# Kernel optimization log

Measured on AMD Instinct MI355X. Metric: run time of the kernel, lower is better.

The kernel has to match this reference:

```python
import jax, jax.numpy as jnp
import numpy as np

NUM_SAMPLED = 8192
NUM_CLASSES = 50000
DIM = 512
BATCH = 8192


def _log_uniform_expected(ids, num_sampled, num_classes):
    # log-uniform sampler probability: P(c) = (log(c+2) - log(c+1)) / log(V+1)
    c = ids.astype(jnp.float32)
    p = (jnp.log(c + 2.0) - jnp.log(c + 1.0)) / jnp.log(float(num_classes + 1))
    # expected count under unique sampling of num_sampled candidates (as in TF)
    return -jnp.expm1(float(num_sampled) * jnp.log1p(-p))


def setup_inputs() -> dict:
    key = jax.random.key(0)
    k1, k2, k3, k4, k5 = jax.random.split(key, 5)
    inputs = jax.random.normal(k1, (BATCH, DIM), jnp.float32)
    labels = jax.random.randint(k2, (BATCH, 1), 0, NUM_CLASSES)
    kernel = jax.random.uniform(k3, (NUM_CLASSES, DIM), jnp.float32, -0.05, 0.05)
    bias = jax.random.uniform(k4, (NUM_CLASSES,), jnp.float32, -0.05, 0.05)
    sampled = jax.random.randint(k5, (NUM_SAMPLED,), 0, NUM_CLASSES)
    return {"inputs": inputs, "labels": labels, "kernel": kernel,
            "bias": bias, "sampled": sampled}


def reference(inputs, labels, kernel, bias, sampled):
    # tf.nn.sampled_softmax_loss (train branch), num_true=1,
    # log-uniform sampler, remove_accidental_hits=True.
    labels_flat = labels[:, 0]

    # true logits: gather one weight row per example, dot with input
    w_true = kernel[labels_flat]                      # [B, D]
    b_true = bias[labels_flat]                        # [B]
    true_logits = jnp.einsum('bd,bd->b', inputs, w_true) + b_true
    true_logits = true_logits - jnp.log(
        _log_uniform_expected(labels_flat, NUM_SAMPLED, NUM_CLASSES))

    # sampled logits: gather S candidate rows, small matmul [B,D]x[D,S]
    w_samp = kernel[sampled]                          # [S, D]
    b_samp = bias[sampled]                            # [S]
    sampled_logits = jnp.einsum('bd,sd->bs', inputs, w_samp) + b_samp[None, :]
    sampled_logits = sampled_logits - jnp.log(
        _log_uniform_expected(sampled, NUM_SAMPLED, NUM_CLASSES))

    # remove accidental hits: mask sampled candidates that equal the true label
    hits = labels_flat[:, None] == sampled[None, :]   # [B, S]
    sampled_logits = jnp.where(hits, -1e9, sampled_logits)

    # softmax CE with the true class at column 0
    logits = jnp.concatenate([true_logits[:, None], sampled_logits], axis=1)
    loss = jax.nn.logsumexp(logits, axis=1) - logits[:, 0]  # [B]
    return loss
```

## Files before the change

kernel.cpp:

```cpp
#include <hip/hip_runtime.h>
#include <hip/hip_bf16.h>
#include <cstdint>
#include <cstddef>

#define BATCH   8192
#define NSAMP   8192
#define DIM     512
#define NCLASS  50000
#define HBINS   50176

typedef __attribute__((ext_vector_type(8))) short bf16x8;
typedef __attribute__((ext_vector_type(4))) float f32x4;

__device__ __forceinline__ float neg_log_expected(int c) {
    double p = log1p(1.0 / (double)(c + 1)) / log((double)(NCLASS + 1));
    double e = -expm1((double)NSAMP * log1p(-p));
    return (float)(-log(e));
}

__device__ __forceinline__ unsigned short f2bf(float f) {
    __hip_bfloat16 h = __float2bfloat16(f);
    return *reinterpret_cast<unsigned short*>(&h);
}

__device__ __forceinline__ void gload_lds16(const void* g, void* l) {
    __builtin_amdgcn_global_load_lds(
        (const __attribute__((address_space(1))) void*)g,
        (__attribute__((address_space(3))) void*)l, 16, 0, 0);
}

__global__ void k_zero(int* __restrict__ hist) {
    hist[blockIdx.x * 1024 + threadIdx.x] = 0;
}
__global__ void k_hist(const int* __restrict__ sampled, int* __restrict__ hist) {
    atomicAdd(&hist[sampled[blockIdx.x * 1024 + threadIdx.x]], 1);
}
__global__ void k_scan1(const int* __restrict__ hist, int* __restrict__ btot) {
    int b = blockIdx.x, t = threadIdx.x;
    int c = b * 196 + t;
    int x = (t < 196 && c < NCLASS && hist[c] > 0) ? 1 : 0;
    int lane = t & 63, wv = t >> 6;
    #pragma unroll
    for (int off = 32; off; off >>= 1) x += __shfl_down(x, off, 64);
    __shared__ int ws[4];
    if (lane == 0) ws[wv] = x;
    __syncthreads();
    if (t == 0) btot[b] = ws[0] + ws[1] + ws[2] + ws[3];
}
__global__ void k_scan2(const int* __restrict__ btot, int* __restrict__ boff,
                        int* __restrict__ meta) {
    int t = threadIdx.x;
    int v = btot[t];
    int lane = t & 63, wv = t >> 6;
    int x = v;
    #pragma unroll
    for (int off = 1; off < 64; off <<= 1) {
        int y = __shfl_up(x, off, 64);
        if (lane >= off) x += y;
    }
    __shared__ int ws[4];
    if (lane == 63) ws[wv] = x;
    __syncthreads();
    int base = 0;
    for (int w = 0; w < wv; ++w) base += ws[w];
    boff[t] = base + x - v;
    if (t == 255) {
        int D = base + x;
        meta[0] = D;
        meta[1] = (D + 127) & ~127;
    }
}
__global__ void k_scatter(const int* __restrict__ hist, const int* __restrict__ boff,
                          int* __restrict__ didx) {
    int b = blockIdx.x, t = threadIdx.x;
    int c = b * 196 + t;
    int ind = (t < 196 && c < NCLASS && hist[c] > 0) ? 1 : 0;
    int lane = t & 63, wv = t >> 6;
    int x = ind;
    #pragma unroll
    for (int off = 1; off < 64; off <<= 1) {
        int y = __shfl_up(x, off, 64);
        if (lane >= off) x += y;
    }
    __shared__ int ws[4];
    if (lane == 63) ws[wv] = x;
    __syncthreads();
    int base = boff[b];
    for (int w = 0; w < wv; ++w) base += ws[w];
    if (ind) didx[base + x - 1] = c;
}

__global__ void k_prep(const float* __restrict__ inputs, const int* __restrict__ labels,
                       const float* __restrict__ W, const float* __restrict__ bias,
                       const int* __restrict__ hist, const int* __restrict__ didx,
                       const int* __restrict__ meta,
                       __hip_bfloat16* __restrict__ Abf, __hip_bfloat16* __restrict__ Bbf,
                       float* __restrict__ adj,
                       float* __restrict__ true_logit, float* __restrict__ row_sum) {
    int bid = blockIdx.x;
    int t   = threadIdx.x;
    if (bid < BATCH) {
        int row = bid;
        float4 v = reinterpret_cast<const float4*>(inputs + (size_t)row * DIM)[t];
        ushort4 u;
        u.x = f2bf(v.x); u.y = f2bf(v.y); u.z = f2bf(v.z); u.w = f2bf(v.w);
        reinterpret_cast<ushort4*>(Abf + (size_t)row * DIM)[t] = u;

        int lbl = labels[row];
        float4 w = reinterpret_cast<const float4*>(W + (size_t)lbl * DIM)[t];
        float dot = v.x * w.x + v.y * w.y + v.z * w.z + v.w * w.w;
        #pragma unroll
        for (int off = 32; off; off >>= 1) dot += __shfl_down(dot, off, 64);
        __shared__ float red[2];
        if ((t & 63) == 0) red[t >> 6] = dot;
        __syncthreads();
        if (t == 0) {
            float tl = red[0] + red[1] + bias[lbl] + neg_log_expected(lbl);
            true_logit[row] = tl;
            row_sum[row]    = (1.0f - (float)hist[lbl]) * __expf(tl);
        }
    } else {
        int s = bid - BATCH;
        int D = meta[0], padD = meta[1];
        if (s >= padD) return;
        if (s < D) {
            int idx = didx[s];
            float4 v = reinterpret_cast<const float4*>(W + (size_t)idx * DIM)[t];
            ushort4 u;
            u.x = f2bf(v.x); u.y = f2bf(v.y); u.z = f2bf(v.z); u.w = f2bf(v.w);
            reinterpret_cast<ushort4*>(Bbf + (size_t)s * DIM)[t] = u;
            if (t == 0)
                adj[s] = bias[idx] + neg_log_expected(idx) + logf((float)hist[idx]);
        } else {
            ushort4 z; z.x = z.y = z.z = z.w = 0;
            reinterpret_cast<ushort4*>(Bbf + (size_t)s * DIM)[t] = z;
            if (t == 0) adj[s] = -100000.0f;
        }
    }
}

__global__ __launch_bounds__(256, 4) void k_gemm(
    const __hip_bfloat16* __restrict__ A, const __hip_bfloat16* __restrict__ B,
    const float* __restrict__ adj, const int* __restrict__ labels,
    const int* __restrict__ meta, float* __restrict__ row_sum) {
    __shared__ alignas(16) __hip_bfloat16 Asm[2][128 * 32];
    __shared__ alignas(16) __hip_bfloat16 Bsm[2][128 * 32];
    __shared__ float tsum[2][128];

    const int tid  = threadIdx.x;
    const int wave = tid >> 6;
    const int lane = tid & 63;
    const int wr   = wave >> 1;
    const int wc   = wave & 1;

    const int bid  = blockIdx.x;
    const int xcd  = bid & 7;
    const int u    = bid >> 3;
    const int rb   = xcd * 8 + (u & 7);
    const int cgrp = u >> 3;
    const int brow = rb * 128;

    const int nct = meta[1] >> 7;
    const int ntl = (nct > cgrp) ? (((nct - cgrp - 1) >> 4) + 1) : 0;
    if (ntl == 0) return;
    const int nsteps = ntl << 4;

    const int srow = lane >> 2;
    const int sg   = (lane & 3) ^ ((lane >> 3) & 3);
    const int rsel = lane & 15;
    const int koff = ((lane >> 4) ^ ((lane >> 1) & 3)) * 8;

    f32x4 acc[4][4];
    #pragma unroll
    for (int m = 0; m < 4; ++m)
        #pragma unroll
        for (int n = 0; n < 4; ++n)
            acc[m][n] = (f32x4){0.f, 0.f, 0.f, 0.f};

    auto stage = [&](int g) {
        const int buf = g & 1, t = g >> 4, kt = g & 15;
        const int bcol = (cgrp + t * 16) << 7;
        #pragma unroll
        for (int i = 0; i < 2; ++i) {
            const __hip_bfloat16* gA =
                A + (size_t)(brow + wave * 32 + i * 16 + srow) * DIM + kt * 32 + sg * 8;
            gload_lds16(gA, &Asm[buf][(wave * 32 + i * 16) * 32]);
            const __hip_bfloat16* gB =
                B + (size_t)(bcol + wave * 32 + i * 16 + srow) * DIM + kt * 32 + sg * 8;
            gload_lds16(gB, &Bsm[buf][(wave * 32 + i * 16) * 32]);
        }
    };

    auto body = [&](int buf) {
        bf16x8 a[4], b[4];
        #pragma unroll
        for (int m = 0; m < 4; ++m)
            a[m] = *reinterpret_cast<const bf16x8*>(
                &Asm[buf][(wr * 64 + m * 16 + rsel) * 32 + koff]);
        #pragma unroll
        for (int n = 0; n < 4; ++n)
            b[n] = *reinterpret_cast<const bf16x8*>(
                &Bsm[buf][(wc * 64 + n * 16 + rsel) * 32 + koff]);
        #pragma unroll
        for (int m = 0; m < 4; ++m)
            #pragma unroll
            for (int n = 0; n < 4; ++n)
                acc[m][n] = __builtin_amdgcn_mfma_f32_16x16x32_bf16(a[m], b[n], acc[m][n], 0, 0, 0);
    };

    auto epi = [&](int i) {
        const int bcol = (cgrp + i * 16) << 7;
        float aadj[4];
        #pragma unroll
        for (int n = 0; n < 4; ++n) aadj[n] = adj[bcol + wc * 64 + n * 16 + rsel];
        #pragma unroll
        for (int m = 0; m < 4; ++m) {
            #pragma unroll
            for (int r = 0; r < 4; ++r) {
                int lr = wr * 64 + m * 16 + (lane >> 4) * 4 + r;
                float part = 0.f;
                #pragma unroll
                for (int n = 0; n < 4; ++n)
                    part += __expf(acc[m][n][r] + aadj[n]);
                part += __shfl_xor(part, 1, 16);
                part += __shfl_xor(part, 2, 16);
                part += __shfl_xor(part, 4, 16);
                part += __shfl_xor(part, 8, 16);
                if (rsel == 0) tsum[wc][lr] = part;
            }
        }
        __syncthreads();
        if (tid < 128)
            atomicAdd(&row_sum[brow + tid], tsum[0][tid] + tsum[1][tid]);
        #pragma unroll
        for (int m = 0; m < 4; ++m)
            #pragma unroll
            for (int n = 0; n < 4; ++n)
                acc[m][n] = (f32x4){0.f, 0.f, 0.f, 0.f};
    };

    stage(0);
    __syncthreads();

    #pragma unroll 1
    for (int g = 0; g < nsteps; ++g) {
        if (g + 1 < nsteps) stage(g + 1);
        body(g & 1);
        if ((g & 15) == 15) epi(g >> 4);
        __syncthreads();
    }
}

__global__ void k_final(const float* __restrict__ row_sum,
                        const float* __restrict__ true_logit,
                        float* __restrict__ loss) {
    int i = blockIdx.x * blockDim.x + threadIdx.x;
    loss[i] = logf(row_sum[i]) - true_logit[i];
}

extern "C" void kernel_launch(void* const* d_in, const int* in_sizes, int n_in,
                              void* d_out, int out_size, void* d_ws, size_t ws_size,
                              hipStream_t stream) {
    const float* inputs  = (const float*)d_in[0];
    const int*   labels  = (const int*)d_in[1];
    const float* W       = (const float*)d_in[2];
    const float* bias    = (const float*)d_in[3];
    const int*   sampled = (const int*)d_in[4];
    float*       loss    = (float*)d_out;

    char* ws = (char*)d_ws;
    __hip_bfloat16* Abf = (__hip_bfloat16*)ws;
    __hip_bfloat16* Bbf = (__hip_bfloat16*)(ws + (size_t)BATCH * DIM * 2);
    size_t off = (size_t)(BATCH + NSAMP) * DIM * 2;
    float* adj        = (float*)(ws + off);            off += NSAMP * 4;
    float* true_logit = (float*)(ws + off);            off += BATCH * 4;
    float* row_sum    = (float*)(ws + off);            off += BATCH * 4;
    int*   hist       = (int*)(ws + off);              off += HBINS * 4;
    int*   btot       = (int*)(ws + off);              off += 256 * 4;
    int*   boff       = (int*)(ws + off);              off += 256 * 4;
    int*   meta       = (int*)(ws + off);              off += 16;
    int*   didx       = (int*)(ws + off);              off += NSAMP * 4;

    hipLaunchKernelGGL(k_zero,    dim3(HBINS / 1024), dim3(1024), 0, stream, hist);
    hipLaunchKernelGGL(k_hist,    dim3(NSAMP / 1024), dim3(1024), 0, stream, sampled, hist);
    hipLaunchKernelGGL(k_scan1,   dim3(256), dim3(256), 0, stream, hist, btot);
    hipLaunchKernelGGL(k_scan2,   dim3(1),   dim3(256), 0, stream, btot, boff, meta);
    hipLaunchKernelGGL(k_scatter, dim3(256), dim3(256), 0, stream, hist, boff, didx);
    hipLaunchKernelGGL(k_prep,    dim3(BATCH + NSAMP), dim3(128), 0, stream,
                       inputs, labels, W, bias, hist, didx, meta,
                       Abf, Bbf, adj, true_logit, row_sum);
    hipLaunchKernelGGL(k_gemm,    dim3(1024), dim3(256), 0, stream,
                       Abf, Bbf, adj, labels, meta, row_sum);
    hipLaunchKernelGGL(k_final,   dim3(BATCH / 256), dim3(256), 0, stream,
                       row_sum, true_logit, loss);
}
```

Measured before the change: 125.9 us.

## Fuse final loss into GEMM via last-block counter, merge prep rows, memset hist

Removes the separate final kernel by having each GEMM block bump a per-row-block counter after a threadfence; the 16th block to finish reads row_sum atomically and writes the loss. The zeroing kernel is replaced by hipMemsetAsync, which also clears the new counters, and the prep kernel now handles two rows per 256-thread block, halving its block count. This cuts launch overhead and small-kernel tails, at the cost of a global atomic and fence per GEMM block and the requirement that every GEMM block reaches the counter, including those with no tiles.

```diff
diff --git a/kernel.cpp b/kernel.cpp
--- a/kernel.cpp
+++ b/kernel.cpp
@@ -29,9 +29,6 @@
         (__attribute__((address_space(3))) void*)l, 16, 0, 0);
 }
 
-__global__ void k_zero(int* __restrict__ hist) {
-    hist[blockIdx.x * 1024 + threadIdx.x] = 0;
-}
 __global__ void k_hist(const int* __restrict__ sampled, int* __restrict__ hist) {
     atomicAdd(&hist[sampled[blockIdx.x * 1024 + threadIdx.x]], 1);
 }
@@ -90,59 +87,63 @@
     if (ind) didx[base + x - 1] = c;
 }
 
-__global__ void k_prep(const float* __restrict__ inputs, const int* __restrict__ labels,
-                       const float* __restrict__ W, const float* __restrict__ bias,
-                       const int* __restrict__ hist, const int* __restrict__ didx,
-                       const int* __restrict__ meta,
-                       __hip_bfloat16* __restrict__ Abf, __hip_bfloat16* __restrict__ Bbf,
-                       float* __restrict__ adj,
-                       float* __restrict__ true_logit, float* __restrict__ row_sum) {
+__global__ __launch_bounds__(256) void k_prep(
+    const float* __restrict__ inputs, const int* __restrict__ labels,
+    const float* __restrict__ W, const float* __restrict__ bias,
+    const int* __restrict__ hist, const int* __restrict__ didx,
+    const int* __restrict__ meta,
+    __hip_bfloat16* __restrict__ Abf, __hip_bfloat16* __restrict__ Bbf,
+    float* __restrict__ adj,
+    float* __restrict__ true_logit, float* __restrict__ row_sum) {
     int bid = blockIdx.x;
     int t   = threadIdx.x;
-    if (bid < BATCH) {
-        int row = bid;
-        float4 v = reinterpret_cast<const float4*>(inputs + (size_t)row * DIM)[t];
+    int rh  = t >> 7;
+    int t1  = t & 127;
+    if (bid < BATCH / 2) {
+        int row = bid * 2 + rh;
+        float4 v = reinterpret_cast<const float4*>(inputs + (size_t)row * DIM)[t1];
         ushort4 u;
         u.x = f2bf(v.x); u.y = f2bf(v.y); u.z = f2bf(v.z); u.w = f2bf(v.w);
-        reinterpret_cast<ushort4*>(Abf + (size_t)row * DIM)[t] = u;
+        reinterpret_cast<ushort4*>(Abf + (size_t)row * DIM)[t1] = u;
 
         int lbl = labels[row];
-        float4 w = reinterpret_cast<const float4*>(W + (size_t)lbl * DIM)[t];
+        float4 w = reinterpret_cast<const float4*>(W + (size_t)lbl * DIM)[t1];
         float dot = v.x * w.x + v.y * w.y + v.z * w.z + v.w * w.w;
         #pragma unroll
         for (int off = 32; off; off >>= 1) dot += __shfl_down(dot, off, 64);
-        __shared__ float red[2];
+        __shared__ float red[4];
         if ((t & 63) == 0) red[t >> 6] = dot;
         __syncthreads();
-        if (t == 0) {
-            float tl = red[0] + red[1] + bias[lbl] + neg_log_expected(lbl);
+        if (t1 == 0) {
+            float tl = red[rh * 2] + red[rh * 2 + 1] + bias[lbl] + neg_log_expected(lbl);
             true_logit[row] = tl;
             row_sum[row]    = (1.0f - (float)hist[lbl]) * __expf(tl);
         }
     } else {
-        int s = bid - BATCH;
+        int s = (bid - BATCH / 2) * 2 + rh;
         int D = meta[0], padD = meta[1];
         if (s >= padD) return;
         if (s < D) {
             int idx = didx[s];
-            float4 v = reinterpret_cast<const float4*>(W + (size_t)idx * DIM)[t];
+            float4 v = reinterpret_cast<const float4*>(W + (size_t)idx * DIM)[t1];
             ushort4 u;
             u.x = f2bf(v.x); u.y = f2bf(v.y); u.z = f2bf(v.z); u.w = f2bf(v.w);
-            reinterpret_cast<ushort4*>(Bbf + (size_t)s * DIM)[t] = u;
-            if (t == 0)
+            reinterpret_cast<ushort4*>(Bbf + (size_t)s * DIM)[t1] = u;
+            if (t1 == 0)
                 adj[s] = bias[idx] + neg_log_expected(idx) + logf((float)hist[idx]);
         } else {
             ushort4 z; z.x = z.y = z.z = z.w = 0;
-            reinterpret_cast<ushort4*>(Bbf + (size_t)s * DIM)[t] = z;
-            if (t == 0) adj[s] = -100000.0f;
+            reinterpret_cast<ushort4*>(Bbf + (size_t)s * DIM)[t1] = z;
+            if (t1 == 0) adj[s] = -100000.0f;
         }
     }
 }
 
 __global__ __launch_bounds__(256, 4) void k_gemm(
     const __hip_bfloat16* __restrict__ A, const __hip_bfloat16* __restrict__ B,
-    const float* __restrict__ adj, const int* __restrict__ labels,
-    const int* __restrict__ meta, float* __restrict__ row_sum) {
+    const float* __restrict__ adj, const int* __restrict__ meta,
+    float* __restrict__ row_sum, const float* __restrict__ true_logit,
+    float* __restrict__ loss, int* __restrict__ cnt) {
     __shared__ alignas(16) __hip_bfloat16 Asm[2][128 * 32];
     __shared__ alignas(16) __hip_bfloat16 Bsm[2][128 * 32];
     __shared__ float tsum[2][128];
@@ -162,7 +163,6 @@
 
     const int nct = meta[1] >> 7;
     const int ntl = (nct > cgrp) ? (((nct - cgrp - 1) >> 4) + 1) : 0;
-    if (ntl == 0) return;
     const int nsteps = ntl << 4;
 
     const int srow = lane >> 2;
@@ -170,92 +170,97 @@
     const int rsel = lane & 15;
     const int koff = ((lane >> 4) ^ ((lane >> 1) & 3)) * 8;
 
-    f32x4 acc[4][4];
-    #pragma unroll
-    for (int m = 0; m < 4; ++m)
-        #pragma unroll
-        for (int n = 0; n < 4; ++n)
-            acc[m][n] = (f32x4){0.f, 0.f, 0.f, 0.f};
-
-    auto stage = [&](int g) {
-        const int buf = g & 1, t = g >> 4, kt = g & 15;
-        const int bcol = (cgrp + t * 16) << 7;
-        #pragma unroll
-        for (int i = 0; i < 2; ++i) {
-            const __hip_bfloat16* gA =
-                A + (size_t)(brow + wave * 32 + i * 16 + srow) * DIM + kt * 32 + sg * 8;
-            gload_lds16(gA, &Asm[buf][(wave * 32 + i * 16) * 32]);
-            const __hip_bfloat16* gB =
-                B + (size_t)(bcol + wave * 32 + i * 16 + srow) * DIM + kt * 32 + sg * 8;
-            gload_lds16(gB, &Bsm[buf][(wave * 32 + i * 16) * 32]);
-        }
-    };
-
-    auto body = [&](int buf) {
-        bf16x8 a[4], b[4];
+    if (nsteps > 0) {
+        f32x4 acc[4][4];
         #pragma unroll
         for (int m = 0; m < 4; ++m)
-            a[m] = *reinterpret_cast<const bf16x8*>(
-                &Asm[buf][(wr * 64 + m * 16 + rsel) * 32 + koff]);
-        #pragma unroll
-        for (int n = 0; n < 4; ++n)
-            b[n] = *reinterpret_cast<const bf16x8*>(
-                &Bsm[buf][(wc * 64 + n * 16 + rsel) * 32 + koff]);
-        #pragma unroll
-        for (int m = 0; m < 4; ++m)
             #pragma unroll
             for (int n = 0; n < 4; ++n)
-                acc[m][n] = __builtin_amdgcn_mfma_f32_16x16x32_bf16(a[m], b[n], acc[m][n], 0, 0, 0);
-    };
-
-    auto epi = [&](int i) {
-        const int bcol = (cgrp + i * 16) << 7;
-        float aadj[4];
-        #pragma unroll
-        for (int n = 0; n < 4; ++n) aadj[n] = adj[bcol + wc * 64 + n * 16 + rsel];
-        #pragma unroll
-        for (int m = 0; m < 4; ++m) {
-            #pragma unroll
-            for (int r = 0; r < 4; ++r) {
-                int lr = wr * 64 + m * 16 + (lane >> 4) * 4 + r;
-                float part = 0.f;
+                acc[m][n] = (f32x4){0.f, 0.f, 0.f, 0.f};
+
+        auto stage = [&](int g) {
+            const int buf = g & 1, t = g >> 4, kt = g & 15;
+            const int bcol = (cgrp + t * 16) << 7;
+            #pragma unroll
+            for (int i = 0; i < 2; ++i) {
+                const __hip_bfloat16* gA =
+                    A + (size_t)(brow + wave * 32 + i * 16 + srow) * DIM + kt * 32 + sg * 8;
+                gload_lds16(gA, &Asm[buf][(wave * 32 + i * 16) * 32]);
+                const __hip_bfloat16* gB =
+                    B + (size_t)(bcol + wave * 32 + i * 16 + srow) * DIM + kt * 32 + sg * 8;
+                gload_lds16(gB, &Bsm[buf][(wave * 32 + i * 16) * 32]);
+            }
+        };
+
+        auto body = [&](int buf) {
+            bf16x8 a[4], b[4];
+            #pragma unroll
+            for (int m = 0; m < 4; ++m)
+                a[m] = *reinterpret_cast<const bf16x8*>(
+                    &Asm[buf][(wr * 64 + m * 16 + rsel) * 32 + koff]);
+            #pragma unroll
+            for (int n = 0; n < 4; ++n)
+                b[n] = *reinterpret_cast<const bf16x8*>(
+                    &Bsm[buf][(wc * 64 + n * 16 + rsel) * 32 + koff]);
+            #pragma unroll
+            for (int m = 0; m < 4; ++m)
                 #pragma unroll
                 for (int n = 0; n < 4; ++n)
-                    part += __expf(acc[m][n][r] + aadj[n]);
-                part += __shfl_xor(part, 1, 16);
-                part += __shfl_xor(part, 2, 16);
-                part += __shfl_xor(part, 4, 16);
-                part += __shfl_xor(part, 8, 16);
-                if (rsel == 0) tsum[wc][lr] = part;
+                    acc[m][n] = __builtin_amdgcn_mfma_f32_16x16x32_bf16(a[m], b[n], acc[m][n], 0, 0, 0);
+        };
+
+        auto epi = [&](int i) {
+            const int bcol = (cgrp + i * 16) << 7;
+            float aadj[4];
+            #pragma unroll
+            for (int n = 0; n < 4; ++n) aadj[n] = adj[bcol + wc * 64 + n * 16 + rsel];
+            #pragma unroll
+            for (int m = 0; m < 4; ++m) {
+                #pragma unroll
+                for (int r = 0; r < 4; ++r) {
+                    int lr = wr * 64 + m * 16 + (lane >> 4) * 4 + r;
+                    float part = 0.f;
+                    #pragma unroll
+                    for (int n = 0; n < 4; ++n)
+                        part += __expf(acc[m][n][r] + aadj[n]);
+                    part += __shfl_xor(part, 1, 16);
+                    part += __shfl_xor(part, 2, 16);
+                    part += __shfl_xor(part, 4, 16);
+                    part += __shfl_xor(part, 8, 16);
+                    if (rsel == 0) tsum[wc][lr] = part;
+                }
             }
+            __syncthreads();
+            if (tid < 128)
+                atomicAdd(&row_sum[brow + tid], tsum[0][tid] + tsum[1][tid]);
+            #pragma unroll
+            for (int m = 0; m < 4; ++m)
+                #pragma unroll
+                for (int n = 0; n < 4; ++n)
+                    acc[m][n] = (f32x4){0.f, 0.f, 0.f, 0.f};
+        };
+
+        stage(0);
+        __syncthreads();
+
+        #pragma unroll 1
+        for (int g = 0; g < nsteps; ++g) {
+            if (g + 1 < nsteps) stage(g + 1);
+            body(g & 1);
+            if ((g & 15) == 15) epi(g >> 4);
+            __syncthreads();
         }
-        __syncthreads();
-        if (tid < 128)
-            atomicAdd(&row_sum[brow + tid], tsum[0][tid] + tsum[1][tid]);
-        #pragma unroll
-        for (int m = 0; m < 4; ++m)
-            #pragma unroll
-            for (int n = 0; n < 4; ++n)
-                acc[m][n] = (f32x4){0.f, 0.f, 0.f, 0.f};
-    };
-
-    stage(0);
+    }
+
+    __threadfence();
+    __shared__ int done;
+    if (tid == 0) done = atomicAdd(&cnt[rb], 1);
     __syncthreads();
-
-    #pragma unroll 1
-    for (int g = 0; g < nsteps; ++g) {
-        if (g + 1 < nsteps) stage(g + 1);
-        body(g & 1);
-        if ((g & 15) == 15) epi(g >> 4);
-        __syncthreads();
-    }
-}
-
-__global__ void k_final(const float* __restrict__ row_sum,
-                        const float* __restrict__ true_logit,
-                        float* __restrict__ loss) {
-    int i = blockIdx.x * blockDim.x + threadIdx.x;
-    loss[i] = logf(row_sum[i]) - true_logit[i];
+    if (done == 15 && tid < 128) {
+        int r = brow + tid;
+        float rs = atomicAdd(&row_sum[r], 0.0f);
+        loss[r] = logf(rs) - true_logit[r];
+    }
 }
 
 extern "C" void kernel_launch(void* const* d_in, const int* in_sizes, int n_in,
@@ -276,21 +281,20 @@
     float* true_logit = (float*)(ws + off);            off += BATCH * 4;
     float* row_sum    = (float*)(ws + off);            off += BATCH * 4;
     int*   hist       = (int*)(ws + off);              off += HBINS * 4;
+    int*   cnt        = (int*)(ws + off);              off += 64 * 4;
     int*   btot       = (int*)(ws + off);              off += 256 * 4;
     int*   boff       = (int*)(ws + off);              off += 256 * 4;
     int*   meta       = (int*)(ws + off);              off += 16;
     int*   didx       = (int*)(ws + off);              off += NSAMP * 4;
 
-    hipLaunchKernelGGL(k_zero,    dim3(HBINS / 1024), dim3(1024), 0, stream, hist);
+    hipMemsetAsync(hist, 0, (size_t)HBINS * 4 + 64 * 4, stream);
     hipLaunchKernelGGL(k_hist,    dim3(NSAMP / 1024), dim3(1024), 0, stream, sampled, hist);
     hipLaunchKernelGGL(k_scan1,   dim3(256), dim3(256), 0, stream, hist, btot);
     hipLaunchKernelGGL(k_scan2,   dim3(1),   dim3(256), 0, stream, btot, boff, meta);
     hipLaunchKernelGGL(k_scatter, dim3(256), dim3(256), 0, stream, hist, boff, didx);
-    hipLaunchKernelGGL(k_prep,    dim3(BATCH + NSAMP), dim3(128), 0, stream,
+    hipLaunchKernelGGL(k_prep,    dim3(BATCH), dim3(256), 0, stream,
                        inputs, labels, W, bias, hist, didx, meta,
                        Abf, Bbf, adj, true_logit, row_sum);
     hipLaunchKernelGGL(k_gemm,    dim3(1024), dim3(256), 0, stream,
-                       Abf, Bbf, adj, labels, meta, row_sum);
-    hipLaunchKernelGGL(k_final,   dim3(BATCH / 256), dim3(256), 0, stream,
-                       row_sum, true_logit, loss);
-}
+                       Abf, Bbf, adj, meta, row_sum, true_logit, loss, cnt);
+}
```

Result: slower. 189.0 us (+50.1%).
